# Optimization experiments

Measured on AMD Instinct MI355X. Metric: run time of the kernel, lower is better.

The kernel has to match this reference:

```python
import jax, jax.numpy as jnp
import numpy as np

N_ITER = 64   # projected-subgradient iterations of the batched DRO QP solver
LR0 = 0.05    # base step size (diminishing 1/sqrt(t))


def project_simplex(v):
    # Euclidean projection onto {z >= 0, sum z = 1} (sort-based, O(n log n))
    n = v.shape[0]
    u = jnp.sort(v)[::-1]
    css = jnp.cumsum(u) - 1.0
    k = jnp.arange(1, n + 1, dtype=v.dtype)
    cond = (u - css / k) > 0          # prefix-true pattern
    idx = jnp.sum(cond.astype(jnp.int32)) - 1
    theta = jnp.take(css, idx) / jnp.take(k, idx)
    return jnp.maximum(v - theta, 0.0)


def _dro_obj(z, c, lam, ep, y_hat, rho):
    # Tractable TV-DRO counterpart (Ben-Tal et al. 2013) with eta and obj_aux
    # eliminated analytically:
    #   obj_i* = max(-lam, u_i - eta),  u_i = (ep_i.z - c)^2
    #   feasibility: eta >= max_i u_i - lam; objective nondecreasing in eta
    #   => eta* = max_i u_i - lam
    s = ep @ z - c                     # (n_obs,)
    u = s * s
    umax = jnp.max(u)
    inner = jnp.mean(jnp.maximum(-lam, u - umax + lam))
    return (umax - lam) + rho * lam + inner - jnp.dot(y_hat, z)


_grad_obj = jax.grad(_dro_obj, argnums=(0, 1, 2))


def _solve_one(y_hat, ep, rho):
    # Projected subgradient descent on (z in simplex, c free, lam >= 0)
    n_y = y_hat.shape[0]
    z0 = jnp.full((n_y,), 1.0 / n_y, y_hat.dtype)
    c0 = jnp.mean(ep @ z0)
    lam0 = jnp.asarray(1.0, y_hat.dtype)

    def step(carry, t):
        z, c, lam = carry
        gz, gc, glam = _grad_obj(z, c, lam, ep, y_hat, rho)
        lr = LR0 / jnp.sqrt(t + 1.0)
        z = project_simplex(z - lr * gz)
        c = c - lr * gc
        lam = jnp.maximum(lam - lr * glam, 0.0)
        return (z, c, lam), None

    (z, _, _), _ = jax.lax.scan(step, (z0, c0, lam0),
                                jnp.arange(N_ITER, dtype=y_hat.dtype))
    return z


def setup_inputs() -> dict:
    key = jax.random.key(0)
    kx, ky, kw, kb = jax.random.split(key, 4)
    n_obs, n_x, n_y = 2048, 128, 64
    X = jax.random.normal(kx, (n_obs, n_x), jnp.float32)
    Y = jax.random.normal(ky, (n_obs, n_y), jnp.float32)
    W = jax.random.normal(kw, (n_y, n_x), jnp.float32) / np.sqrt(n_x).astype(np.float32)
    b = jax.random.normal(kb, (n_y,), jnp.float32) * 0.01
    rho = jnp.array([0.1], jnp.float32)
    return {"X": X, "Y": Y, "rho": rho, "W": W, "b": b}


def reference(X, Y, rho, W, b):
    # prediction layer: per-sample linear predict (vectorized over n_obs)
    Y_hat = X @ W.T + b                        # (n_obs, n_y)
    ep = Y - Y_hat                             # residuals, shared by all solves
    # batched DRO solve: one convex problem per scenario y_hat_t (vmapped)
    Z_star = jax.vmap(lambda yh: _solve_one(yh, ep, rho[0]))(Y_hat)
    Z_star = jax.lax.stop_gradient(Z_star)     # torch code detaches z_t
    return Z_star, Y_hat
```

## Files before the change

### kernel.cpp

```cpp
#include <hip/hip_runtime.h>

#define NOBS 2048
#define NX   128
#define NY   64
#define BS   8
#define NT   1024
#define NWAVE (NT / 64)
#define NITER 64

template <int CTRL>
__device__ __forceinline__ float dpp_f(float x) {
    return __int_as_float(__builtin_amdgcn_update_dpp(
        0, __float_as_int(x), CTRL, 0xf, 0xf, true));
}
__device__ __forceinline__ float wave_sum64(float v) {
    v += dpp_f<0x111>(v);
    v += dpp_f<0x112>(v);
    v += dpp_f<0x114>(v);
    v += dpp_f<0x118>(v);
    v += dpp_f<0x142>(v);
    v += dpp_f<0x143>(v);
    return v;
}
__device__ __forceinline__ float wave_max64_nonneg(float v) {
    v = fmaxf(v, dpp_f<0x111>(v));
    v = fmaxf(v, dpp_f<0x112>(v));
    v = fmaxf(v, dpp_f<0x114>(v));
    v = fmaxf(v, dpp_f<0x118>(v));
    v = fmaxf(v, dpp_f<0x142>(v));
    v = fmaxf(v, dpp_f<0x143>(v));
    return v;
}

__global__ __launch_bounds__(256) void prep_kernel(
    const float* __restrict__ X, const float* __restrict__ Y,
    const float* __restrict__ W, const float* __restrict__ b,
    float* __restrict__ yhat_out, float* __restrict__ ep, float* __restrict__ epsum)
{
    __shared__ float Xs[4][NX];
    const int t = threadIdx.x;
    const int row0 = blockIdx.x * 4;
    for (int f = t; f < 4 * NX; f += 256)
        Xs[f >> 7][f & 127] = X[(row0 + (f >> 7)) * NX + (f & 127)];
    __syncthreads();

    const int k = t & 63;
    const int r = t >> 6;
    const float4* W4 = reinterpret_cast<const float4*>(W + k * NX);
    const float4* X4 = reinterpret_cast<const float4*>(&Xs[r][0]);
    float acc = 0.f;
    #pragma unroll
    for (int x = 0; x < NX / 4; ++x) {
        float4 wv = W4[x];
        float4 xv = X4[x];
        acc += wv.x * xv.x + wv.y * xv.y + wv.z * xv.z + wv.w * xv.w;
    }
    const float yh = acc + b[k];
    const int i = row0 + r;
    yhat_out[i * NY + k] = yh;
    const float e = Y[i * NY + k] - yh;
    ep[i * NY + k] = e;

    float se = wave_sum64(e);
    if ((t & 63) == 63) atomicAdd(epsum, se);
}

__global__ __launch_bounds__(NT, 4) void solve_kernel(
    const float* __restrict__ ep, const float* __restrict__ yhat,
    const float* __restrict__ epsum, const float* __restrict__ rho_p,
    float* __restrict__ zout)
{
    __shared__ float Zs[BS][NY];
    __shared__ float Yh[BS][NY];
    __shared__ float V[NOBS][BS];
    __shared__ float Rpart[NWAVE][NY][BS];
    __shared__ float Rr[NY][BS];
    __shared__ float redBuf[NWAVE][32];
    __shared__ float scal[32];
    __shared__ float umaxS[BS], cS[BS], lamS[BS], gcS[BS], glamS[BS], wAS[BS];

    const int t = threadIdx.x;
    const int lane = t & 63;
    const int wv = t >> 6;
    const int sc0 = blockIdx.x * BS;
    const float rho = rho_p[0];

    if (t < BS * NY) {
        const int j = t >> 6, k = t & 63;
        Yh[j][k] = yhat[(sc0 + j) * NY + k];
        Zs[j][k] = 1.0f / 64.0f;
    }
    if (t < BS) {
        cS[t] = epsum[0] * (1.0f / 131072.0f);
        lamS[t] = 1.0f;
    }
    __syncthreads();

    const int i0 = t;
    const int i1 = t + NT;
    const float4* ep4 = reinterpret_cast<const float4*>(ep);

    for (int it = 0; it < NITER; ++it) {
        const float lr = 0.05f / sqrtf((float)it + 1.0f);

        float s0[BS], s1[BS];
        #pragma unroll
        for (int j = 0; j < BS; ++j) { s0[j] = 0.f; s1[j] = 0.f; }
        #pragma unroll 4
        for (int k4 = 0; k4 < NY / 4; ++k4) {
            const float4 ea = ep4[i0 * (NY / 4) + k4];
            const float4 eb = ep4[i1 * (NY / 4) + k4];
            #pragma unroll
            for (int j = 0; j < BS; ++j) {
                const float4 zv = *reinterpret_cast<const float4*>(&Zs[j][k4 * 4]);
                s0[j] += ea.x * zv.x + ea.y * zv.y + ea.z * zv.z + ea.w * zv.w;
                s1[j] += eb.x * zv.x + eb.y * zv.y + eb.z * zv.z + eb.w * zv.w;
            }
        }
        float lamR[BS];
        #pragma unroll
        for (int j = 0; j < BS; ++j) {
            const float cj = cS[j];
            lamR[j] = lamS[j];
            s0[j] -= cj; s1[j] -= cj;
        }

        #pragma unroll
        for (int j = 0; j < BS; ++j) {
            float pm = fmaxf(s0[j] * s0[j], s1[j] * s1[j]);
            pm = wave_max64_nonneg(pm);
            if (lane == 63) redBuf[wv][j] = pm;
        }
        __syncthreads();
        if (t < BS) {
            float m = redBuf[0][t];
            #pragma unroll
            for (int w = 1; w < NWAVE; ++w) m = fmaxf(m, redBuf[w][t]);
            umaxS[t] = m;
        }
        __syncthreads();

        #pragma unroll
        for (int j = 0; j < BS; ++j) {
            const float um = umaxS[j], lm = lamR[j];
            float pa = 0.f, pe = 0.f, pas = 0.f, pes = 0.f;
            {
                const float s = s0[j], u = s * s;
                const float x = (u - um) + lm;
                const float a = (x > -lm) ? 1.0f : ((x == -lm) ? 0.5f : 0.0f);
                const float e = (u == um) ? 1.0f : 0.0f;
                pa += a; pe += e; pas += a * s; pes += e * s;
            }
            {
                const float s = s1[j], u = s * s;
                const float x = (u - um) + lm;
                const float a = (x > -lm) ? 1.0f : ((x == -lm) ? 0.5f : 0.0f);
                const float e = (u == um) ? 1.0f : 0.0f;
                pa += a; pe += e; pas += a * s; pes += e * s;
            }
            pa = wave_sum64(pa); pe = wave_sum64(pe);
            pas = wave_sum64(pas); pes = wave_sum64(pes);
            if (lane == 63) {
                redBuf[wv][j] = pa;       redBuf[wv][8 + j] = pe;
                redBuf[wv][16 + j] = pas; redBuf[wv][24 + j] = pes;
            }
        }
        __syncthreads();
        if (t < 32) {
            float ssum = 0.f;
            #pragma unroll
            for (int w = 0; w < NWAVE; ++w) ssum += redBuf[w][t];
            scal[t] = ssum;
        }
        __syncthreads();
        if (t < BS) {
            const int j = t;
            const float sumA = scal[j], sumEq = scal[8 + j];
            const float sumAS = scal[16 + j], sumEqS = scal[24 + j];
            const float abar = sumA * (1.0f / (float)NOBS);
            const float wA = (1.0f - abar) / sumEq;
            wAS[j] = wA;
            gcS[j] = -2.0f * (sumAS * (1.0f / (float)NOBS) + wA * sumEqS);
            glamS[j] = (rho - 2.0f) + 2.0f * abar;
        }
        __syncthreads();

        {
            float v0[BS], v1[BS];
            #pragma unroll
            for (int j = 0; j < BS; ++j) {
                const float um = umaxS[j], lm = lamR[j], wA = wAS[j];
                {
                    const float s = s0[j], u = s * s;
                    const float x = (u - um) + lm;
                    const float a = (x > -lm) ? 1.0f : ((x == -lm) ? 0.5f : 0.0f);
                    const float e = (u == um) ? 1.0f : 0.0f;
                    v0[j] = (a * (1.0f / (float)NOBS) + e * wA) * s;
                }
                {
                    const float s = s1[j], u = s * s;
                    const float x = (u - um) + lm;
                    const float a = (x > -lm) ? 1.0f : ((x == -lm) ? 0.5f : 0.0f);
                    const float e = (u == um) ? 1.0f : 0.0f;
                    v1[j] = (a * (1.0f / (float)NOBS) + e * wA) * s;
                }
            }
            *reinterpret_cast<float4*>(&V[i0][0]) = make_float4(v0[0], v0[1], v0[2], v0[3]);
            *reinterpret_cast<float4*>(&V[i0][4]) = make_float4(v0[4], v0[5], v0[6], v0[7]);
            *reinterpret_cast<float4*>(&V[i1][0]) = make_float4(v1[0], v1[1], v1[2], v1[3]);
            *reinterpret_cast<float4*>(&V[i1][4]) = make_float4(v1[4], v1[5], v1[6], v1[7]);
        }
        __syncthreads();

        {
            float rp[BS];
            #pragma unroll
            for (int j = 0; j < BS; ++j) rp[j] = 0.f;
            const int ibeg = wv * (NOBS / NWAVE);
            #pragma unroll 4
            for (int ii = 0; ii < NOBS / NWAVE; ++ii) {
                const int i = ibeg + ii;
                const float e = ep[i * NY + lane];
                const float4 va = *reinterpret_cast<const float4*>(&V[i][0]);
                const float4 vb = *reinterpret_cast<const float4*>(&V[i][4]);
                rp[0] += e * va.x; rp[1] += e * va.y; rp[2] += e * va.z; rp[3] += e * va.w;
                rp[4] += e * vb.x; rp[5] += e * vb.y; rp[6] += e * vb.z; rp[7] += e * vb.w;
            }
            *reinterpret_cast<float4*>(&Rpart[wv][lane][0]) = make_float4(rp[0], rp[1], rp[2], rp[3]);
            *reinterpret_cast<float4*>(&Rpart[wv][lane][4]) = make_float4(rp[4], rp[5], rp[6], rp[7]);
        }
        __syncthreads();
        if (t < NY * BS) {
            const int k = t >> 3, j = t & 7;
            float ssum = 0.f;
            #pragma unroll
            for (int w = 0; w < NWAVE; ++w) ssum += Rpart[w][k][j];
            Rr[k][j] = ssum;
        }
        __syncthreads();

        if (wv < BS) {
            const int j = wv, k = lane;
            const float r = Rr[k][j];
            const float gz = 2.0f * r - Yh[j][k];
            const float vz = Zs[j][k] - lr * gz;

            float sv = vz;
            #pragma unroll
            for (int sz = 2; sz <= 64; sz <<= 1) {
                #pragma unroll
                for (int st = sz >> 1; st > 0; st >>= 1) {
                    const float other = __shfl_xor(sv, st, 64);
                    const bool desc = ((lane & sz) == 0);
                    const bool lower = ((lane & st) == 0);
                    const float mx = fmaxf(sv, other), mn = fminf(sv, other);
                    sv = (lower == desc) ? mx : mn;
                }
            }
            float css = sv;
            #pragma unroll
            for (int off = 1; off < 64; off <<= 1) {
                const float nb = __shfl_up(css, off, 64);
                if (lane >= off) css += nb;
            }
            css -= 1.0f;
            const bool cond = (sv - css / (float)(lane + 1)) > 0.0f;
            const unsigned long long bal = __ballot(cond);
            const int idx = __popcll(bal) - 1;
            const float cssIdx = __shfl(css, idx, 64);
            const float theta = cssIdx / (float)(idx + 1);
            Zs[j][k] = fmaxf(vz - theta, 0.0f);
            if (lane == 0) {
                cS[j] = cS[j] - lr * gcS[j];
                lamS[j] = fmaxf(lamS[j] - lr * glamS[j], 0.0f);
            }
        }
        __syncthreads();
    }

    if (t < BS * NY) {
        const int j = t >> 6, k = t & 63;
        zout[(sc0 + j) * NY + k] = Zs[j][k];
    }
}

extern "C" void kernel_launch(void* const* d_in, const int* in_sizes, int n_in,
                              void* d_out, int out_size, void* d_ws, size_t ws_size,
                              hipStream_t stream) {
    const float* X   = (const float*)d_in[0];
    const float* Y   = (const float*)d_in[1];
    const float* rho = (const float*)d_in[2];
    const float* W   = (const float*)d_in[3];
    const float* b   = (const float*)d_in[4];

    float* out   = (float*)d_out;
    float* zout  = out;
    float* yhat  = out + NOBS * NY;
    float* ep    = (float*)d_ws;
    float* epsum = ep + NOBS * NY;

    hipMemsetAsync(epsum, 0, sizeof(float), stream);
    prep_kernel<<<NOBS / 4, 256, 0, stream>>>(X, Y, W, b, yhat, ep, epsum);
    solve_kernel<<<NOBS / BS, NT, 0, stream>>>(ep, yhat, epsum, rho, zout);
}
```

Baseline: 2.172 ms.

## Replace serial per-block reductions with redundant per-wave reductions to cut barriers

Each wave now redundantly reduces the cross-wave partials for umax, the four gradient sums and the R vector itself, using lane-indexed loads and shuffles. Previously a handful of threads did each reduction into shared memory, and every one needed an extra __syncthreads. That removes four block-wide barriers per iteration and several shared scalars. The c/lambda update moves into wave 0 earlier in the iteration. This should be safe because the other waves read cS/lamS only at the start of the next iteration, after later barriers. The cost is duplicated reduction work across all 16 waves and more register pressure.

```diff
diff --git a/kernel.cpp b/kernel.cpp
--- a/kernel.cpp
+++ b/kernel.cpp
@@ -74,10 +74,9 @@
     __shared__ float Yh[BS][NY];
     __shared__ float V[NOBS][BS];
     __shared__ float Rpart[NWAVE][NY][BS];
-    __shared__ float Rr[NY][BS];
-    __shared__ float redBuf[NWAVE][32];
-    __shared__ float scal[32];
-    __shared__ float umaxS[BS], cS[BS], lamS[BS], gcS[BS], glamS[BS], wAS[BS];
+    __shared__ float redM[NWAVE][BS];
+    __shared__ float red2[NWAVE][4 * BS];
+    __shared__ float cS[BS], lamS[BS];
 
     const int t = threadIdx.x;
     const int lane = t & 63;
@@ -129,20 +128,22 @@
         for (int j = 0; j < BS; ++j) {
             float pm = fmaxf(s0[j] * s0[j], s1[j] * s1[j]);
             pm = wave_max64_nonneg(pm);
-            if (lane == 63) redBuf[wv][j] = pm;
-        }
-        __syncthreads();
-        if (t < BS) {
-            float m = redBuf[0][t];
-            #pragma unroll
-            for (int w = 1; w < NWAVE; ++w) m = fmaxf(m, redBuf[w][t]);
-            umaxS[t] = m;
-        }
-        __syncthreads();
+            if (lane == 63) redM[wv][j] = pm;
+        }
+        __syncthreads();
+
+        float mv = 0.f;
+        if (lane < BS) {
+            #pragma unroll
+            for (int w = 0; w < NWAVE; ++w) mv = fmaxf(mv, redM[w][lane]);
+        }
+        float umaxR[BS];
+        #pragma unroll
+        for (int j = 0; j < BS; ++j) umaxR[j] = __shfl(mv, j, 64);
 
         #pragma unroll
         for (int j = 0; j < BS; ++j) {
-            const float um = umaxS[j], lm = lamR[j];
+            const float um = umaxR[j], lm = lamR[j];
             float pa = 0.f, pe = 0.f, pas = 0.f, pes = 0.f;
             {
                 const float s = s0[j], u = s * s;
@@ -161,35 +162,42 @@
             pa = wave_sum64(pa); pe = wave_sum64(pe);
             pas = wave_sum64(pas); pes = wave_sum64(pes);
             if (lane == 63) {
-                redBuf[wv][j] = pa;       redBuf[wv][8 + j] = pe;
-                redBuf[wv][16 + j] = pas; redBuf[wv][24 + j] = pes;
-            }
-        }
-        __syncthreads();
-        if (t < 32) {
-            float ssum = 0.f;
-            #pragma unroll
-            for (int w = 0; w < NWAVE; ++w) ssum += redBuf[w][t];
-            scal[t] = ssum;
-        }
-        __syncthreads();
-        if (t < BS) {
-            const int j = t;
-            const float sumA = scal[j], sumEq = scal[8 + j];
-            const float sumAS = scal[16 + j], sumEqS = scal[24 + j];
+                red2[wv][j]          = pa;  red2[wv][BS + j]     = pe;
+                red2[wv][2 * BS + j] = pas; red2[wv][3 * BS + j] = pes;
+            }
+        }
+        __syncthreads();
+
+        float sv = 0.f;
+        if (lane < 4 * BS) {
+            #pragma unroll
+            for (int w = 0; w < NWAVE; ++w) sv += red2[w][lane];
+        }
+        float wAr[BS], gcKeep = 0.f, glamKeep = 0.f;
+        #pragma unroll
+        for (int j = 0; j < BS; ++j) {
+            const float sumA   = __shfl(sv, j, 64);
+            const float sumEq  = __shfl(sv, BS + j, 64);
+            const float sumAS  = __shfl(sv, 2 * BS + j, 64);
+            const float sumEqS = __shfl(sv, 3 * BS + j, 64);
             const float abar = sumA * (1.0f / (float)NOBS);
             const float wA = (1.0f - abar) / sumEq;
-            wAS[j] = wA;
-            gcS[j] = -2.0f * (sumAS * (1.0f / (float)NOBS) + wA * sumEqS);
-            glamS[j] = (rho - 2.0f) + 2.0f * abar;
-        }
-        __syncthreads();
+            wAr[j] = wA;
+            if (lane == j) {
+                gcKeep   = -2.0f * (sumAS * (1.0f / (float)NOBS) + wA * sumEqS);
+                glamKeep = (rho - 2.0f) + 2.0f * abar;
+            }
+        }
+        if (wv == 0 && lane < BS) {
+            cS[lane]  = cS[lane] - lr * gcKeep;
+            lamS[lane] = fmaxf(lamS[lane] - lr * glamKeep, 0.0f);
+        }
 
         {
             float v0[BS], v1[BS];
             #pragma unroll
             for (int j = 0; j < BS; ++j) {
-                const float um = umaxS[j], lm = lamR[j], wA = wAS[j];
+                const float um = umaxR[j], lm = lamR[j], wA = wAr[j];
                 {
                     const float s = s0[j], u = s * s;
                     const float x = (u - um) + lm;
@@ -230,50 +238,40 @@
             *reinterpret_cast<float4*>(&Rpart[wv][lane][4]) = make_float4(rp[4], rp[5], rp[6], rp[7]);
         }
         __syncthreads();
-        if (t < NY * BS) {
-            const int k = t >> 3, j = t & 7;
-            float ssum = 0.f;
-            #pragma unroll
-            for (int w = 0; w < NWAVE; ++w) ssum += Rpart[w][k][j];
-            Rr[k][j] = ssum;
-        }
-        __syncthreads();
 
         if (wv < BS) {
             const int j = wv, k = lane;
-            const float r = Rr[k][j];
+            float r = 0.f;
+            #pragma unroll
+            for (int w = 0; w < NWAVE; ++w) r += Rpart[w][k][j];
             const float gz = 2.0f * r - Yh[j][k];
             const float vz = Zs[j][k] - lr * gz;
 
-            float sv = vz;
+            float sv2 = vz;
             #pragma unroll
             for (int sz = 2; sz <= 64; sz <<= 1) {
                 #pragma unroll
                 for (int st = sz >> 1; st > 0; st >>= 1) {
-                    const float other = __shfl_xor(sv, st, 64);
+                    const float other = __shfl_xor(sv2, st, 64);
                     const bool desc = ((lane & sz) == 0);
                     const bool lower = ((lane & st) == 0);
-                    const float mx = fmaxf(sv, other), mn = fminf(sv, other);
-                    sv = (lower == desc) ? mx : mn;
+                    const float mx = fmaxf(sv2, other), mn = fminf(sv2, other);
+                    sv2 = (lower == desc) ? mx : mn;
                 }
             }
-            float css = sv;
+            float css = sv2;
             #pragma unroll
             for (int off = 1; off < 64; off <<= 1) {
                 const float nb = __shfl_up(css, off, 64);
                 if (lane >= off) css += nb;
             }
             css -= 1.0f;
-            const bool cond = (sv - css / (float)(lane + 1)) > 0.0f;
+            const bool cond = (sv2 - css / (float)(lane + 1)) > 0.0f;
             const unsigned long long bal = __ballot(cond);
             const int idx = __popcll(bal) - 1;
             const float cssIdx = __shfl(css, idx, 64);
             const float theta = cssIdx / (float)(idx + 1);
             Zs[j][k] = fmaxf(vz - theta, 0.0f);
-            if (lane == 0) {
-                cS[j] = cS[j] - lr * gcS[j];
-                lamS[j] = fmaxf(lamS[j] - lr * glamS[j], 0.0f);
-            }
         }
         __syncthreads();
     }
```

Result: slower. 2.231 ms (+2.7%).
